# Kernel tuning notes

Measured on AMD Instinct MI355X. Metric: run time of the kernel, lower is better.

## Reference

```python
import jax, jax.numpy as jnp
import numpy as np

B, S, D = 2, 2048, 1024
N_EXP, TOP_K = 8, 2
CAP_FACTOR = 1.25

def setup_inputs() -> dict:
    key = jax.random.key(0)
    k1, k2 = jax.random.split(key)
    x = jax.random.normal(k1, (B, S, D), dtype=jnp.float32)
    W_gate = jax.random.normal(k2, (N_EXP, D), dtype=jnp.float32) * (1.0 / np.sqrt(D))
    return {"x": x, "W_gate": W_gate}

def reference(x, W_gate):
    Bq, Sq, d = x.shape
    N = Bq * Sq                      # num_tokens
    n_exp = W_gate.shape[0]
    top_k = TOP_K
    cap = int(N * top_k * CAP_FACTOR / n_exp)  # exp_capacity (static)

    x_flat = x.reshape(N, d)
    logits = x_flat @ W_gate.T                      # [N, n_exp]
    top_vals, top_idx = jax.lax.top_k(logits, top_k)  # [N, k]
    gates = jax.nn.softmax(top_vals, axis=-1)       # [N, k]

    # Serial token-major, k-minor assignment order == flatten row-major.
    e_flat = top_idx.reshape(-1)                    # [N*k]
    oh = jax.nn.one_hot(e_flat, n_exp, dtype=jnp.int32)
    # position within expert = # earlier slots routed to same expert
    pos = (jnp.cumsum(oh, axis=0) - oh)[jnp.arange(N * top_k), e_flat]
    pos_safe = jnp.where(pos < cap, pos, cap)       # cap -> out-of-bounds -> dropped

    tok = jnp.arange(N * top_k) // top_k            # owning token per slot
    g_flat = gates.reshape(-1)

    exp_mask = jnp.zeros((N, n_exp, cap), jnp.float32)
    exp_mask = exp_mask.at[tok, e_flat, pos_safe].set(g_flat, mode='drop')

    exp_batches = jnp.zeros((n_exp, cap, d), jnp.float32)
    exp_batches = exp_batches.at[e_flat, pos_safe].set(x_flat[tok], mode='drop')

    return gates, exp_mask, exp_batches
```

## Files before the change

### kernel.cpp

```cpp
#include <hip/hip_runtime.h>
#include <math.h>

#define NTOK   4096
#define DIM    1024
#define NEXP   8
#define CAP    1280

#define OUT_MASK_OFF   ((size_t)NTOK*2)
#define OUT_BATCH_OFF  (OUT_MASK_OFF + (size_t)NTOK*NEXP*CAP)

typedef float f4 __attribute__((ext_vector_type(4)));

__global__ __launch_bounds__(256) void gate_kernel(
    const float* __restrict__ x, const float* __restrict__ Wg,
    float* __restrict__ gates_out,
    int* __restrict__ e0a, int* __restrict__ e1a,
    float* __restrict__ g0a, float* __restrict__ g1a)
{
    const int wave = threadIdx.x >> 6;
    const int lane = threadIdx.x & 63;
    const int t    = blockIdx.x * 4 + wave;

    const f4* xr = (const f4*)(x + (size_t)t * DIM);
    f4 xv[4];
#pragma unroll
    for (int p = 0; p < 4; ++p) xv[p] = xr[p * 64 + lane];

    float acc[NEXP];
#pragma unroll
    for (int e = 0; e < NEXP; ++e) {
        const f4* wr = (const f4*)(Wg + (size_t)e * DIM);
        float a = 0.f;
#pragma unroll
        for (int p = 0; p < 4; ++p) {
            const f4 w = wr[p * 64 + lane];
            a += xv[p].x * w.x + xv[p].y * w.y + xv[p].z * w.z + xv[p].w * w.w;
        }
        acc[e] = a;
    }

#pragma unroll
    for (int off = 32; off >= 1; off >>= 1) {
#pragma unroll
        for (int e = 0; e < NEXP; ++e)
            acc[e] += __shfl_xor(acc[e], off);
    }

    if (lane == 0) {
        float best = -INFINITY, second = -INFINITY;
        int b0 = 0, b1 = 0;
#pragma unroll
        for (int e = 0; e < NEXP; ++e) {
            const float v = acc[e];
            if (v > best)        { second = best; b1 = b0; best = v; b0 = e; }
            else if (v > second) { second = v; b1 = e; }
        }
        const float e1v = __expf(second - best);
        const float inv = 1.0f / (1.0f + e1v);
        const float g0 = inv, g1 = e1v * inv;

        gates_out[(size_t)t * 2]     = g0;
        gates_out[(size_t)t * 2 + 1] = g1;
        e0a[t] = b0; e1a[t] = b1;
        g0a[t] = g0; g1a[t] = g1;
    }
}

__global__ __launch_bounds__(256) void scan_kernel(
    const int* __restrict__ e0a, const int* __restrict__ e1a,
    int* __restrict__ pos0a, int* __restrict__ pos1a,
    int* __restrict__ inv_out)
{
    __shared__ int invs[NEXP * CAP];
    __shared__ unsigned wtot[4][4];

    const int tid  = threadIdx.x;
    const int wave = tid >> 6;
    const int lane = tid & 63;

    for (int i = tid; i < NEXP * CAP; i += 256) invs[i] = -1;

    const int tok0 = tid * 16;
    int ea[16], eb[16];
    {
        const int4* va = (const int4*)(e0a + tok0);
        const int4* vb = (const int4*)(e1a + tok0);
#pragma unroll
        for (int q = 0; q < 4; ++q) {
            int4 a = va[q], b = vb[q];
            ea[4*q] = a.x; ea[4*q+1] = a.y; ea[4*q+2] = a.z; ea[4*q+3] = a.w;
            eb[4*q] = b.x; eb[4*q+1] = b.y; eb[4*q+2] = b.z; eb[4*q+3] = b.w;
        }
    }

    int local[NEXP];
#pragma unroll
    for (int e = 0; e < NEXP; ++e) local[e] = 0;
#pragma unroll
    for (int j = 0; j < 16; ++j) { local[ea[j]]++; local[eb[j]]++; }

    unsigned pk[4];
#pragma unroll
    for (int q = 0; q < 4; ++q)
        pk[q] = (unsigned)local[2*q] | ((unsigned)local[2*q+1] << 16);
    const unsigned my0 = pk[0], my1 = pk[1], my2 = pk[2], my3 = pk[3];

#pragma unroll
    for (int off = 1; off < 64; off <<= 1) {
        unsigned n0 = __shfl_up((int)pk[0], off);
        unsigned n1 = __shfl_up((int)pk[1], off);
        unsigned n2 = __shfl_up((int)pk[2], off);
        unsigned n3 = __shfl_up((int)pk[3], off);
        if (lane >= off) { pk[0] += n0; pk[1] += n1; pk[2] += n2; pk[3] += n3; }
    }

    if (lane == 63) {
#pragma unroll
        for (int q = 0; q < 4; ++q) wtot[wave][q] = pk[q];
    }
    __syncthreads();

#pragma unroll
    for (int w = 0; w < 4; ++w) {
        if (w < wave) {
            pk[0] += wtot[w][0]; pk[1] += wtot[w][1];
            pk[2] += wtot[w][2]; pk[3] += wtot[w][3];
        }
    }
    pk[0] -= my0; pk[1] -= my1; pk[2] -= my2; pk[3] -= my3;

    int run[NEXP];
#pragma unroll
    for (int q = 0; q < 4; ++q) {
        run[2*q]   = (int)(pk[q] & 0xFFFFu);
        run[2*q+1] = (int)(pk[q] >> 16);
    }

    int p0r[16], p1r[16];
#pragma unroll
    for (int j = 0; j < 16; ++j) {
        const int tok = tok0 + j;
        int e = ea[j];
        int p = run[e]++;
        p0r[j] = p;
        if (p < CAP) invs[e * CAP + p] = tok;
        e = eb[j];
        p = run[e]++;
        p1r[j] = p;
        if (p < CAP) invs[e * CAP + p] = tok;
    }

#pragma unroll
    for (int q = 0; q < 4; ++q) {
        ((int4*)(pos0a + tok0))[q] = make_int4(p0r[4*q], p0r[4*q+1], p0r[4*q+2], p0r[4*q+3]);
        ((int4*)(pos1a + tok0))[q] = make_int4(p1r[4*q], p1r[4*q+1], p1r[4*q+2], p1r[4*q+3]);
    }
    __syncthreads();

    for (int i = tid; i < NEXP * CAP / 4; i += 256)
        ((int4*)inv_out)[i] = ((const int4*)invs)[i];
}

#define BATCH_BLOCKS 2560
__global__ __launch_bounds__(256) void writer_kernel(
    const int* __restrict__ e0a, const int* __restrict__ e1a,
    const int* __restrict__ pos0a, const int* __restrict__ pos1a,
    const float* __restrict__ g0a, const float* __restrict__ g1a,
    const int* __restrict__ inv, const float* __restrict__ x,
    float* __restrict__ mask_out, float* __restrict__ batch_out)
{
    const int tid = threadIdx.x;

    if (blockIdx.x < BATCH_BLOCKS) {
        const int base = blockIdx.x * 4;
#pragma unroll
        for (int i = 0; i < 4; ++i) {
            const int row = base + i;
            const int tok = inv[row];
            f4 v = (f4)(0.f);
            if (tok >= 0)
                v = ((const f4*)(x + (size_t)tok * DIM))[tid];
            __builtin_nontemporal_store(v, (f4*)(batch_out + (size_t)row * DIM) + tid);
        }
    } else {
        const int t = blockIdx.x - BATCH_BLOCKS;

        const int   e0 = e0a[t], e1 = e1a[t];
        const int   p0 = pos0a[t], p1 = pos1a[t];
        const float g0 = g0a[t],  g1 = g1a[t];

        f4* dst = (f4*)(mask_out + (size_t)t * NEXP * CAP);

#pragma unroll
        for (int i = 0; i < 10; ++i) {
            const int idx = tid + i * 256;
            const int e   = idx / (CAP / 4);
            const int c   = (idx - e * (CAP / 4)) * 4;

            f4 v = (f4)(0.f);
            if (e == e0) {
                if (p0 == c)     v.x = g0;
                if (p0 == c + 1) v.y = g0;
                if (p0 == c + 2) v.z = g0;
                if (p0 == c + 3) v.w = g0;
            }
            if (e == e1) {
                if (p1 == c)     v.x = g1;
                if (p1 == c + 1) v.y = g1;
                if (p1 == c + 2) v.z = g1;
                if (p1 == c + 3) v.w = g1;
            }
            __builtin_nontemporal_store(v, dst + idx);
        }
    }
}

extern "C" void kernel_launch(void* const* d_in, const int* in_sizes, int n_in,
                              void* d_out, int out_size, void* d_ws, size_t ws_size,
                              hipStream_t stream)
{
    const float* x  = (const float*)d_in[0];
    const float* Wg = (const float*)d_in[1];

    float* out   = (float*)d_out;
    float* gates = out;
    float* mask  = out + OUT_MASK_OFF;
    float* batch = out + OUT_BATCH_OFF;

    int* wsi = (int*)d_ws;
    int*   e0a  = wsi;
    int*   e1a  = wsi + NTOK;
    float* g0a  = (float*)(wsi + 2 * NTOK);
    float* g1a  = (float*)(wsi + 3 * NTOK);
    int*   p0a  = wsi + 4 * NTOK;
    int*   p1a  = wsi + 5 * NTOK;
    int*   inv  = wsi + 6 * NTOK;

    gate_kernel  <<<NTOK / 4, 256, 0, stream>>>(x, Wg, gates, e0a, e1a, g0a, g1a);
    scan_kernel  <<<1, 256, 0, stream>>>(e0a, e1a, p0a, p1a, inv);
    writer_kernel<<<BATCH_BLOCKS + NTOK, 256, 0, stream>>>(
        e0a, e1a, p0a, p1a, g0a, g1a, inv, x, mask, batch);
}
```

Baseline: 238.5 us.

## Fuse gating and scan kernels via last-block atomic counter

Merges the gate and single-block scan kernels into one launch. Each block computes gates for its tokens, then increments a global counter, and the last block to finish runs the prefix scan. This removes one kernel launch and its dependency gap, but adds a memset launch plus fence and atomic overhead. Every gate block now also reserves the large shared array, which may lower occupancy. The writer kernel also loads its four inverse indices as one vector load.

```diff
diff --git a/kernel.cpp b/kernel.cpp
--- a/kernel.cpp
+++ b/kernel.cpp
@@ -5,78 +5,85 @@
 #define DIM    1024
 #define NEXP   8
 #define CAP    1280
+#define GATE_BLOCKS (NTOK / 4)
 
 #define OUT_MASK_OFF   ((size_t)NTOK*2)
 #define OUT_BATCH_OFF  (OUT_MASK_OFF + (size_t)NTOK*NEXP*CAP)
 
 typedef float f4 __attribute__((ext_vector_type(4)));
 
-__global__ __launch_bounds__(256) void gate_kernel(
+__global__ __launch_bounds__(256) void gate_scan_kernel(
     const float* __restrict__ x, const float* __restrict__ Wg,
     float* __restrict__ gates_out,
     int* __restrict__ e0a, int* __restrict__ e1a,
-    float* __restrict__ g0a, float* __restrict__ g1a)
-{
-    const int wave = threadIdx.x >> 6;
-    const int lane = threadIdx.x & 63;
-    const int t    = blockIdx.x * 4 + wave;
-
-    const f4* xr = (const f4*)(x + (size_t)t * DIM);
-    f4 xv[4];
-#pragma unroll
-    for (int p = 0; p < 4; ++p) xv[p] = xr[p * 64 + lane];
-
-    float acc[NEXP];
-#pragma unroll
-    for (int e = 0; e < NEXP; ++e) {
-        const f4* wr = (const f4*)(Wg + (size_t)e * DIM);
-        float a = 0.f;
-#pragma unroll
-        for (int p = 0; p < 4; ++p) {
-            const f4 w = wr[p * 64 + lane];
-            a += xv[p].x * w.x + xv[p].y * w.y + xv[p].z * w.z + xv[p].w * w.w;
-        }
-        acc[e] = a;
-    }
-
-#pragma unroll
-    for (int off = 32; off >= 1; off >>= 1) {
-#pragma unroll
-        for (int e = 0; e < NEXP; ++e)
-            acc[e] += __shfl_xor(acc[e], off);
-    }
-
-    if (lane == 0) {
-        float best = -INFINITY, second = -INFINITY;
-        int b0 = 0, b1 = 0;
-#pragma unroll
-        for (int e = 0; e < NEXP; ++e) {
-            const float v = acc[e];
-            if (v > best)        { second = best; b1 = b0; best = v; b0 = e; }
-            else if (v > second) { second = v; b1 = e; }
-        }
-        const float e1v = __expf(second - best);
-        const float inv = 1.0f / (1.0f + e1v);
-        const float g0 = inv, g1 = e1v * inv;
-
-        gates_out[(size_t)t * 2]     = g0;
-        gates_out[(size_t)t * 2 + 1] = g1;
-        e0a[t] = b0; e1a[t] = b1;
-        g0a[t] = g0; g1a[t] = g1;
-    }
-}
-
-__global__ __launch_bounds__(256) void scan_kernel(
-    const int* __restrict__ e0a, const int* __restrict__ e1a,
+    float* __restrict__ g0a, float* __restrict__ g1a,
     int* __restrict__ pos0a, int* __restrict__ pos1a,
-    int* __restrict__ inv_out)
+    int* __restrict__ inv_out, int* __restrict__ flag)
 {
     __shared__ int invs[NEXP * CAP];
     __shared__ unsigned wtot[4][4];
+    __shared__ int is_last;
 
     const int tid  = threadIdx.x;
     const int wave = tid >> 6;
     const int lane = tid & 63;
+
+    {
+        const int t = blockIdx.x * 4 + wave;
+        const f4* xr = (const f4*)(x + (size_t)t * DIM);
+        f4 xv[4];
+#pragma unroll
+        for (int p = 0; p < 4; ++p) xv[p] = xr[p * 64 + lane];
+
+        float acc[NEXP];
+#pragma unroll
+        for (int e = 0; e < NEXP; ++e) {
+            const f4* wr = (const f4*)(Wg + (size_t)e * DIM);
+            float a = 0.f;
+#pragma unroll
+            for (int p = 0; p < 4; ++p) {
+                const f4 w = wr[p * 64 + lane];
+                a += xv[p].x * w.x + xv[p].y * w.y + xv[p].z * w.z + xv[p].w * w.w;
+            }
+            acc[e] = a;
+        }
+
+#pragma unroll
+        for (int off = 32; off >= 1; off >>= 1) {
+#pragma unroll
+            for (int e = 0; e < NEXP; ++e)
+                acc[e] += __shfl_xor(acc[e], off);
+        }
+
+        if (lane == 0) {
+            float best = -INFINITY, second = -INFINITY;
+            int b0 = 0, b1 = 0;
+#pragma unroll
+            for (int e = 0; e < NEXP; ++e) {
+                const float v = acc[e];
+                if (v > best)        { second = best; b1 = b0; best = v; b0 = e; }
+                else if (v > second) { second = v; b1 = e; }
+            }
+            const float e1v = __expf(second - best);
+            const float inv = 1.0f / (1.0f + e1v);
+            const float g0 = inv, g1 = e1v * inv;
+
+            gates_out[(size_t)t * 2]     = g0;
+            gates_out[(size_t)t * 2 + 1] = g1;
+            e0a[t] = b0; e1a[t] = b1;
+            g0a[t] = g0; g1a[t] = g1;
+            __threadfence();
+        }
+    }
+    __syncthreads();
+
+    if (tid == 0) {
+        const int old = atomicAdd(flag, 1);
+        is_last = (old == GATE_BLOCKS - 1);
+    }
+    __syncthreads();
+    if (!is_last) return;
+    __threadfence();
 
     for (int i = tid; i < NEXP * CAP; i += 256) invs[i] = -1;
 
@@ -172,15 +179,16 @@
     const int tid = threadIdx.x;
 
     if (blockIdx.x < BATCH_BLOCKS) {
+        const int4 tk = ((const int4*)inv)[blockIdx.x];
+        const int toks[4] = { tk.x, tk.y, tk.z, tk.w };
         const int base = blockIdx.x * 4;
 #pragma unroll
         for (int i = 0; i < 4; ++i) {
-            const int row = base + i;
-            const int tok = inv[row];
+            const int tok = toks[i];
             f4 v = (f4)(0.f);
             if (tok >= 0)
                 v = ((const f4*)(x + (size_t)tok * DIM))[tid];
-            __builtin_nontemporal_store(v, (f4*)(batch_out + (size_t)row * DIM) + tid);
+            __builtin_nontemporal_store(v, (f4*)(batch_out + (size_t)(base + i) * DIM) + tid);
         }
     } else {
         const int t = blockIdx.x - BATCH_BLOCKS;
@@ -235,9 +243,12 @@
     int*   p0a  = wsi + 4 * NTOK;
     int*   p1a  = wsi + 5 * NTOK;
     int*   inv  = wsi + 6 * NTOK;
-
-    gate_kernel  <<<NTOK / 4, 256, 0, stream>>>(x, Wg, gates, e0a, e1a, g0a, g1a);
-    scan_kernel  <<<1, 256, 0, stream>>>(e0a, e1a, p0a, p1a, inv);
+    int*   flag = wsi + 6 * NTOK + NEXP * CAP;
+
+    hipMemsetAsync(flag, 0, sizeof(int), stream);
+
+    gate_scan_kernel<<<GATE_BLOCKS, 256, 0, stream>>>(
+        x, Wg, gates, e0a, e1a, g0a, g1a, p0a, p1a, inv, flag);
     writer_kernel<<<BATCH_BLOCKS + NTOK, 256, 0, stream>>>(
         e0a, e1a, p0a, p1a, g0a, g1a, inv, x, mask, batch);
 }
```

After: 318.4 us. 33.5% more time.

## Zero expert mask with memset and scatter only the nonzero gate entries

Applied to the files above, without the earlier changes.

The per-token mask writer, which generated and stored all 10240 floats of each token's mask row, is replaced by one hipMemsetAsync that clears the whole 168 MB mask. A small set of 16 blocks then scatters the two gate values per token. The batch writer now loads its four inverse-index entries with a single int4 read. The aim is to let the driver's fill path handle the huge zero write instead of compute blocks, at the cost of an extra stream operation and scalar scattered stores that are ordered after the memset.

```diff
diff --git a/kernel.cpp b/kernel.cpp
--- a/kernel.cpp
+++ b/kernel.cpp
@@ -172,46 +172,25 @@
     const int tid = threadIdx.x;
 
     if (blockIdx.x < BATCH_BLOCKS) {
+        const int4 tk = ((const int4*)inv)[blockIdx.x];
+        const int toks[4] = { tk.x, tk.y, tk.z, tk.w };
         const int base = blockIdx.x * 4;
 #pragma unroll
         for (int i = 0; i < 4; ++i) {
-            const int row = base + i;
-            const int tok = inv[row];
+            const int tok = toks[i];
             f4 v = (f4)(0.f);
             if (tok >= 0)
                 v = ((const f4*)(x + (size_t)tok * DIM))[tid];
-            __builtin_nontemporal_store(v, (f4*)(batch_out + (size_t)row * DIM) + tid);
+            __builtin_nontemporal_store(v, (f4*)(batch_out + (size_t)(base + i) * DIM) + tid);
         }
     } else {
-        const int t = blockIdx.x - BATCH_BLOCKS;
-
-        const int   e0 = e0a[t], e1 = e1a[t];
-        const int   p0 = pos0a[t], p1 = pos1a[t];
-        const float g0 = g0a[t],  g1 = g1a[t];
-
-        f4* dst = (f4*)(mask_out + (size_t)t * NEXP * CAP);
-
-#pragma unroll
-        for (int i = 0; i < 10; ++i) {
-            const int idx = tid + i * 256;
-            const int e   = idx / (CAP / 4);
-            const int c   = (idx - e * (CAP / 4)) * 4;
-
-            f4 v = (f4)(0.f);
-            if (e == e0) {
-                if (p0 == c)     v.x = g0;
-                if (p0 == c + 1) v.y = g0;
-                if (p0 == c + 2) v.z = g0;
-                if (p0 == c + 3) v.w = g0;
-            }
-            if (e == e1) {
-                if (p1 == c)     v.x = g1;
-                if (p1 == c + 1) v.y = g1;
-                if (p1 == c + 2) v.z = g1;
-                if (p1 == c + 3) v.w = g1;
-            }
-            __builtin_nontemporal_store(v, dst + idx);
-        }
+        const int t = (blockIdx.x - BATCH_BLOCKS) * 256 + tid;
+        const int e0 = e0a[t], e1 = e1a[t];
+        const int p0 = pos0a[t], p1 = pos1a[t];
+
+        float* row = mask_out + (size_t)t * NEXP * CAP;
+        if (p0 < CAP) row[e0 * CAP + p0] = g0a[t];
+        if (p1 < CAP) row[e1 * CAP + p1] = g1a[t];
     }
 }
 
@@ -236,8 +215,10 @@
     int*   p1a  = wsi + 5 * NTOK;
     int*   inv  = wsi + 6 * NTOK;
 
+    hipMemsetAsync(mask, 0, (size_t)NTOK * NEXP * CAP * sizeof(float), stream);
+
     gate_kernel  <<<NTOK / 4, 256, 0, stream>>>(x, Wg, gates, e0a, e1a, g0a, g1a);
     scan_kernel  <<<1, 256, 0, stream>>>(e0a, e1a, p0a, p1a, inv);
-    writer_kernel<<<BATCH_BLOCKS + NTOK, 256, 0, stream>>>(
+    writer_kernel<<<BATCH_BLOCKS + 16, 256, 0, stream>>>(
         e0a, e1a, p0a, p1a, g0a, g1a, inv, x, mask, batch);
 }
```

New measurement: 229.4 us. 1.04x faster.
